# Optimization experiments

Hardware: AMD Instinct MI355X
Metric: run time of the kernel (lower is better)

Reference implementation:

```python
import jax, jax.numpy as jnp
import numpy as np

F, H, D, A, B = 500, 2000, 64, 64, 4096


def setup_inputs() -> dict:
    key = jax.random.key(0)
    ks = jax.random.split(key, 6)
    values = jax.random.normal(ks[0], (B, F), dtype=jnp.float32)
    feat_emb = jax.random.normal(ks[1], (F, D), dtype=jnp.float32) * 0.02
    hid_emb = jax.random.normal(ks[2], (H, D), dtype=jnp.float32) * 0.02
    Ww = jax.random.normal(ks[3], (2 * D, A), dtype=jnp.float32) * (1.0 / np.sqrt(2 * D))
    bw = jnp.zeros((A,), dtype=jnp.float32)
    Wu = jax.random.normal(ks[4], (A, 1), dtype=jnp.float32) * (1.0 / np.sqrt(A))
    mask = jax.random.bernoulli(ks[5], 0.1, (F, F + H, 1))
    return {"values": values, "feat_emb": feat_emb, "hid_emb": hid_emb,
            "Ww": Ww, "bw": bw, "Wu": Wu, "mask": mask}


def reference(values, feat_emb, hid_emb, Ww, bw, Wu, mask):
    d = feat_emb.shape[1]
    # full embedding matrix: concat(feature, hidden) -> [F+H, d]
    full = jnp.concatenate([feat_emb, hid_emb], axis=0)
    # Dense(tanh) on concat([feat_emb tiled, full tiled], axis=2) == split-weight form:
    # avoids materializing the [F, F+H, 2d] concat tensor (same math).
    W1, W2 = Ww[:d], Ww[d:]
    pre_f = feat_emb @ W1          # [F, A]
    pre_w = full @ W2              # [F+H, A]
    h = jnp.tanh(pre_f[:, None, :] + pre_w[None, :, :] + bw)  # [F, F+H, A]
    score = h @ Wu                 # [F, F+H, 1]
    # masked exp-normalize (not a stable softmax: original uses raw exp)
    score = jnp.where(mask, jnp.exp(score), 0.0)
    ssum = jnp.sum(score, axis=1, keepdims=True)        # [F, 1, 1]
    ssum = jnp.where(ssum == 0, 1.0, ssum)
    attn = score / ssum                                  # [F, F+H, 1]
    context = jnp.sum(attn * full[None, :, :], axis=1)   # [F, d]
    return values @ context                              # [B, d]
```

## Files before the change

kernel.cpp:

```cpp
#include <hip/hip_runtime.h>
#include <cstdint>
#include <cstddef>

#define F_N 500
#define H_N 2000
#define JN  2500
#define D_N 64
#define A_N 64
#define B_N 4096

#define SPLIT  2
#define JCHUNK 1250

__global__ __launch_bounds__(256) void k_pre(
    const float* __restrict__ feat, const float* __restrict__ hid,
    const float* __restrict__ Ww,   const float* __restrict__ bw,
    float* __restrict__ pre_f, float* __restrict__ pre_w,
    float* __restrict__ zero_region)
{
    const int gt = blockIdx.x * 256 + threadIdx.x;
    if (gt < 32512) zero_region[gt] = 0.0f;

    const int lane = threadIdx.x & 63;
    const int wave = threadIdx.x >> 6;
    int row = blockIdx.x * 4 + wave;
    row = __builtin_amdgcn_readfirstlane(row);
    if (row >= F_N + JN) return;

    const float* emb;
    const float* W;
    float*       outp;
    float acc0, acc1 = 0.0f;

    if (row < F_N) {
        emb  = feat + (size_t)row * D_N;
        W    = Ww;
        outp = pre_f + (size_t)row * A_N;
        acc0 = bw[lane];
    } else {
        const int j = row - F_N;
        emb  = (j < F_N) ? (feat + (size_t)j * D_N)
                         : (hid + (size_t)(j - F_N) * D_N);
        W    = Ww + D_N * A_N;
        outp = pre_w + (size_t)j * A_N;
        acc0 = 0.0f;
    }

    #pragma unroll
    for (int d = 0; d < D_N; d += 2) {
        acc0 = fmaf(emb[d],     W[(d    ) * A_N + lane], acc0);
        acc1 = fmaf(emb[d + 1], W[(d + 1) * A_N + lane], acc1);
    }
    outp[lane] = acc0 + acc1;
}

__global__ __launch_bounds__(256) void k_attn(
    const float* __restrict__ feat, const float* __restrict__ hid,
    const float* __restrict__ pre_f, const float* __restrict__ pre_w,
    const float* __restrict__ Wu,   const void* __restrict__ mask,
    float* __restrict__ csum, float* __restrict__ esum)
{
    const int tid  = threadIdx.x;
    const int lane = tid & 63;
    const int wave = tid >> 6;
    const int i    = blockIdx.x >> 1;
    const int sub  = blockIdx.x & 1;
    const int jbase = sub * JCHUNK;

    __shared__ int   list[JCHUNK];
    __shared__ float earr[JCHUNK];
    __shared__ float s_ctx[4][64];
    __shared__ int   nact;

    if (tid == 0) nact = 0;
    __syncthreads();

    const uint32_t* mw = (const uint32_t*)mask;
    const uint32_t probe = mw[lane] | mw[64 + lane] | mw[128 + lane] | mw[192 + lane];
    const bool byteMode = (__ballot(probe > 1u) != 0ull);

    const uint8_t*  mb = (const uint8_t*)mask + (size_t)i * JN + jbase;
    const uint32_t* mi = (const uint32_t*)mask + (size_t)i * JN + jbase;

    for (int t = tid; t < 1280; t += 256) {
        uint32_t m = 0;
        if (t < JCHUNK) m = byteMode ? (uint32_t)mb[t] : mi[t];
        const unsigned long long act = __ballot(m != 0);
        const int cnt = __popcll(act);
        int base = 0;
        if (lane == 0 && cnt) base = atomicAdd(&nact, cnt);
        base = __shfl(base, 0, 64);
        if (m) {
            const int rank = __popcll(act & ((1ull << lane) - 1ull));
            list[base + rank] = jbase + t;
        }
    }
    __syncthreads();
    const int n = nact;

    const float* pf = pre_f + (size_t)i * A_N;
    for (int idx = tid; idx < n; idx += 256) {
        const int j = list[idx];
        const float4* pwj = (const float4*)(pre_w + (size_t)j * A_N);
        float s = 0.0f;
        #pragma unroll
        for (int q = 0; q < 16; ++q) {
            const float4 v = pwj[q];
            const int a = q * 4;
            const float x0 = pf[a + 0] + v.x;
            const float x1 = pf[a + 1] + v.y;
            const float x2 = pf[a + 2] + v.z;
            const float x3 = pf[a + 3] + v.w;
            const float t0 = fmaf(-2.0f, __builtin_amdgcn_rcpf(__expf(2.0f * x0) + 1.0f), 1.0f);
            const float t1 = fmaf(-2.0f, __builtin_amdgcn_rcpf(__expf(2.0f * x1) + 1.0f), 1.0f);
            const float t2 = fmaf(-2.0f, __builtin_amdgcn_rcpf(__expf(2.0f * x2) + 1.0f), 1.0f);
            const float t3 = fmaf(-2.0f, __builtin_amdgcn_rcpf(__expf(2.0f * x3) + 1.0f), 1.0f);
            s = fmaf(Wu[a + 0], t0, s);
            s = fmaf(Wu[a + 1], t1, s);
            s = fmaf(Wu[a + 2], t2, s);
            s = fmaf(Wu[a + 3], t3, s);
        }
        earr[idx] = __expf(s);
    }
    __syncthreads();

    float cacc = 0.0f;
    int idx = wave;
    for (; idx + 12 < n; idx += 16) {
        const float e0 = earr[idx];      const int j0 = list[idx];
        const float e1 = earr[idx + 4];  const int j1 = list[idx + 4];
        const float e2 = earr[idx + 8];  const int j2 = list[idx + 8];
        const float e3 = earr[idx + 12]; const int j3 = list[idx + 12];
        const float* r0 = (j0 < F_N) ? (feat + (size_t)j0 * D_N) : (hid + (size_t)(j0 - F_N) * D_N);
        const float* r1 = (j1 < F_N) ? (feat + (size_t)j1 * D_N) : (hid + (size_t)(j1 - F_N) * D_N);
        const float* r2 = (j2 < F_N) ? (feat + (size_t)j2 * D_N) : (hid + (size_t)(j2 - F_N) * D_N);
        const float* r3 = (j3 < F_N) ? (feat + (size_t)j3 * D_N) : (hid + (size_t)(j3 - F_N) * D_N);
        const float v0 = r0[lane];
        const float v1 = r1[lane];
        const float v2 = r2[lane];
        const float v3 = r3[lane];
        cacc = fmaf(e0, v0, cacc);
        cacc = fmaf(e1, v1, cacc);
        cacc = fmaf(e2, v2, cacc);
        cacc = fmaf(e3, v3, cacc);
    }
    for (; idx < n; idx += 4) {
        const float e = earr[idx];
        const int   j = list[idx];
        const float* row = (j < F_N) ? (feat + (size_t)j * D_N)
                                     : (hid + (size_t)(j - F_N) * D_N);
        cacc = fmaf(e, row[lane], cacc);
    }
    s_ctx[wave][lane] = cacc;
    __syncthreads();

    if (wave == 0) {
        const float c4 = s_ctx[0][lane] + s_ctx[1][lane] + s_ctx[2][lane] + s_ctx[3][lane];
        float ss = 0.0f;
        for (int k = lane; k < n; k += 64) ss += earr[k];
        #pragma unroll
        for (int off = 1; off < 64; off <<= 1) ss += __shfl_xor(ss, off, 64);
        atomicAdd(&csum[(size_t)i * D_N + lane], c4);
        if (lane == 0) atomicAdd(&esum[i], ss);
    }
}

__global__ __launch_bounds__(256) void k_out(
    const float* __restrict__ values, const float* __restrict__ csum,
    const float* __restrict__ esum,   float* __restrict__ out)
{
    const int tid  = threadIdx.x;
    const int lane = tid & 63;
    const int wave = tid >> 6;
    int r0 = blockIdx.x * 8 + wave * 2;
    r0 = __builtin_amdgcn_readfirstlane(r0);

    __shared__ float ctx_l[100 * 64];

    float4 cbuf[7];
    float  ebuf[7];

    float acc0 = 0.0f, acc1 = 0.0f;

    {
        const float4* cp = (const float4*)csum;
        #pragma unroll
        for (int q = 0; q < 7; ++q) {
            const int t = tid + q * 256;
            if (t < 1600) { cbuf[q] = cp[t]; ebuf[q] = esum[t >> 4]; }
        }
    }

    for (int chunk = 0; chunk < 5; ++chunk) {
        __syncthreads();
        {
            float4* cl = (float4*)ctx_l;
            #pragma unroll
            for (int q = 0; q < 7; ++q) {
                const int t = tid + q * 256;
                if (t < 1600) {
                    const float e   = ebuf[q];
                    const float inv = (e == 0.0f) ? 1.0f : __builtin_amdgcn_rcpf(e);
                    float4 c = cbuf[q];
                    c.x *= inv; c.y *= inv; c.z *= inv; c.w *= inv;
                    cl[t] = c;
                }
            }
        }
        __syncthreads();

        if (chunk < 4) {
            const int k0n = (chunk + 1) * 100;
            const float4* cp = (const float4*)(csum + (size_t)k0n * 64);
            #pragma unroll
            for (int q = 0; q < 7; ++q) {
                const int t = tid + q * 256;
                if (t < 1600) { cbuf[q] = cp[t]; ebuf[q] = esum[k0n + (t >> 4)]; }
            }
        }

        const int k0 = chunk * 100;
        const float* v0 = values + (size_t)(r0 + 0) * 500 + k0;
        const float* v1 = values + (size_t)(r0 + 1) * 500 + k0;
        #pragma unroll 10
        for (int k = 0; k < 100; k += 4) {
            const float c0 = ctx_l[(k + 0) * 64 + lane];
            const float c1 = ctx_l[(k + 1) * 64 + lane];
            const float c2 = ctx_l[(k + 2) * 64 + lane];
            const float c3 = ctx_l[(k + 3) * 64 + lane];
            acc0 = fmaf(v0[k + 0], c0, acc0); acc0 = fmaf(v0[k + 1], c1, acc0);
            acc0 = fmaf(v0[k + 2], c2, acc0); acc0 = fmaf(v0[k + 3], c3, acc0);
            acc1 = fmaf(v1[k + 0], c0, acc1); acc1 = fmaf(v1[k + 1], c1, acc1);
            acc1 = fmaf(v1[k + 2], c2, acc1); acc1 = fmaf(v1[k + 3], c3, acc1);
        }
    }

    out[(size_t)(r0 + 0) * 64 + lane] = acc0;
    out[(size_t)(r0 + 1) * 64 + lane] = acc1;
}

extern "C" void kernel_launch(void* const* d_in, const int* in_sizes, int n_in,
                              void* d_out, int out_size, void* d_ws, size_t ws_size,
                              hipStream_t stream)
{
    const float* values = (const float*)d_in[0];
    const float* feat   = (const float*)d_in[1];
    const float* hid    = (const float*)d_in[2];
    const float* Ww     = (const float*)d_in[3];
    const float* bw     = (const float*)d_in[4];
    const float* Wu     = (const float*)d_in[5];
    const void*  mask   = d_in[6];
    float* out = (float*)d_out;

    float* wsf   = (float*)d_ws;
    float* pre_f = wsf;
    float* pre_w = wsf + 32000;
    float* csum  = wsf + 192000;
    float* esum  = wsf + 224000;

    k_pre <<<750,  256, 0, stream>>>(feat, hid, Ww, bw, pre_f, pre_w, csum);
    k_attn<<<1000, 256, 0, stream>>>(feat, hid, pre_f, pre_w, Wu, mask, csum, esum);
    k_out <<<512,  256, 0, stream>>>(values, csum, esum, out);
}
```

Measured before the change: 109.4 us.

## Fuse attention and output kernels into one launch with software grid barrier

After: 267.1 us. +144.2%, slower.

```diff
diff --git a/kernel.cpp b/kernel.cpp
--- a/kernel.cpp
+++ b/kernel.cpp
@@ -11,6 +11,7 @@
 
 #define SPLIT  2
 #define JCHUNK 1250
+#define NBLK   1000
 
 __global__ __launch_bounds__(256) void k_pre(
     const float* __restrict__ feat, const float* __restrict__ hid,
@@ -19,7 +20,7 @@
     float* __restrict__ zero_region)
 {
     const int gt = blockIdx.x * 256 + threadIdx.x;
-    if (gt < 32512) zero_region[gt] = 0.0f;
+    if (gt < 32514) zero_region[gt] = 0.0f;
 
     const int lane = threadIdx.x & 63;
     const int wave = threadIdx.x >> 6;
@@ -54,189 +55,218 @@
     outp[lane] = acc0 + acc1;
 }
 
-__global__ __launch_bounds__(256) void k_attn(
+__device__ __forceinline__ void grid_barrier(int* __restrict__ ctr,
+                                             int* __restrict__ gen,
+                                             int nblocks, bool wait)
+{
+    __syncthreads();
+    if (threadIdx.x == 0) {
+        __threadfence();
+        const int g = __hip_atomic_load(gen, __ATOMIC_RELAXED,
+                                        __HIP_MEMORY_SCOPE_AGENT);
+        const int old = __hip_atomic_fetch_add(ctr, 1, __ATOMIC_ACQ_REL,
+                                               __HIP_MEMORY_SCOPE_AGENT);
+        if (old == nblocks - 1) {
+            __hip_atomic_store(gen, g + 1, __ATOMIC_RELEASE,
+                               __HIP_MEMORY_SCOPE_AGENT);
+        } else if (wait) {
+            while (__hip_atomic_load(gen, __ATOMIC_ACQUIRE,
+                                     __HIP_MEMORY_SCOPE_AGENT) == g) {
+                __builtin_amdgcn_s_sleep(2);
+            }
+        }
+    }
+    if (wait) __syncthreads();
+}
+
+__global__ __launch_bounds__(256, 4) void k_mega(
     const float* __restrict__ feat, const float* __restrict__ hid,
     const float* __restrict__ pre_f, const float* __restrict__ pre_w,
     const float* __restrict__ Wu,   const void* __restrict__ mask,
-    float* __restrict__ csum, float* __restrict__ esum)
+    const float* __restrict__ values,
+    float* __restrict__ csum, float* __restrict__ esum,
+    float* __restrict__ out,  int* __restrict__ bar)
 {
     const int tid  = threadIdx.x;
     const int lane = tid & 63;
     const int wave = tid >> 6;
-    const int i    = blockIdx.x >> 1;
-    const int sub  = blockIdx.x & 1;
-    const int jbase = sub * JCHUNK;
-
-    __shared__ int   list[JCHUNK];
-    __shared__ float earr[JCHUNK];
-    __shared__ float s_ctx[4][64];
-    __shared__ int   nact;
-
-    if (tid == 0) nact = 0;
-    __syncthreads();
-
-    const uint32_t* mw = (const uint32_t*)mask;
-    const uint32_t probe = mw[lane] | mw[64 + lane] | mw[128 + lane] | mw[192 + lane];
-    const bool byteMode = (__ballot(probe > 1u) != 0ull);
-
-    const uint8_t*  mb = (const uint8_t*)mask + (size_t)i * JN + jbase;
-    const uint32_t* mi = (const uint32_t*)mask + (size_t)i * JN + jbase;
-
-    for (int t = tid; t < 1280; t += 256) {
-        uint32_t m = 0;
-        if (t < JCHUNK) m = byteMode ? (uint32_t)mb[t] : mi[t];
-        const unsigned long long act = __ballot(m != 0);
-        const int cnt = __popcll(act);
-        int base = 0;
-        if (lane == 0 && cnt) base = atomicAdd(&nact, cnt);
-        base = __shfl(base, 0, 64);
-        if (m) {
-            const int rank = __popcll(act & ((1ull << lane) - 1ull));
-            list[base + rank] = jbase + t;
-        }
-    }
-    __syncthreads();
-    const int n = nact;
-
-    const float* pf = pre_f + (size_t)i * A_N;
-    for (int idx = tid; idx < n; idx += 256) {
-        const int j = list[idx];
-        const float4* pwj = (const float4*)(pre_w + (size_t)j * A_N);
-        float s = 0.0f;
-        #pragma unroll
-        for (int q = 0; q < 16; ++q) {
-            const float4 v = pwj[q];
-            const int a = q * 4;
-            const float x0 = pf[a + 0] + v.x;
-            const float x1 = pf[a + 1] + v.y;
-            const float x2 = pf[a + 2] + v.z;
-            const float x3 = pf[a + 3] + v.w;
-            const float t0 = fmaf(-2.0f, __builtin_amdgcn_rcpf(__expf(2.0f * x0) + 1.0f), 1.0f);
-            const float t1 = fmaf(-2.0f, __builtin_amdgcn_rcpf(__expf(2.0f * x1) + 1.0f), 1.0f);
-            const float t2 = fmaf(-2.0f, __builtin_amdgcn_rcpf(__expf(2.0f * x2) + 1.0f), 1.0f);
-            const float t3 = fmaf(-2.0f, __builtin_amdgcn_rcpf(__expf(2.0f * x3) + 1.0f), 1.0f);
-            s = fmaf(Wu[a + 0], t0, s);
-            s = fmaf(Wu[a + 1], t1, s);
-            s = fmaf(Wu[a + 2], t2, s);
-            s = fmaf(Wu[a + 3], t3, s);
-        }
-        earr[idx] = __expf(s);
-    }
-    __syncthreads();
-
-    float cacc = 0.0f;
-    int idx = wave;
-    for (; idx + 12 < n; idx += 16) {
-        const float e0 = earr[idx];      const int j0 = list[idx];
-        const float e1 = earr[idx + 4];  const int j1 = list[idx + 4];
-        const float e2 = earr[idx + 8];  const int j2 = list[idx + 8];
-        const float e3 = earr[idx + 12]; const int j3 = list[idx + 12];
-        const float* r0 = (j0 < F_N) ? (feat + (size_t)j0 * D_N) : (hid + (size_t)(j0 - F_N) * D_N);
-        const float* r1 = (j1 < F_N) ? (feat + (size_t)j1 * D_N) : (hid + (size_t)(j1 - F_N) * D_N);
-        const float* r2 = (j2 < F_N) ? (feat + (size_t)j2 * D_N) : (hid + (size_t)(j2 - F_N) * D_N);
-        const float* r3 = (j3 < F_N) ? (feat + (size_t)j3 * D_N) : (hid + (size_t)(j3 - F_N) * D_N);
-        const float v0 = r0[lane];
-        const float v1 = r1[lane];
-        const float v2 = r2[lane];
-        const float v3 = r3[lane];
-        cacc = fmaf(e0, v0, cacc);
-        cacc = fmaf(e1, v1, cacc);
-        cacc = fmaf(e2, v2, cacc);
-        cacc = fmaf(e3, v3, cacc);
-    }
-    for (; idx < n; idx += 4) {
-        const float e = earr[idx];
-        const int   j = list[idx];
-        const float* row = (j < F_N) ? (feat + (size_t)j * D_N)
-                                     : (hid + (size_t)(j - F_N) * D_N);
-        cacc = fmaf(e, row[lane], cacc);
-    }
-    s_ctx[wave][lane] = cacc;
-    __syncthreads();
-
-    if (wave == 0) {
-        const float c4 = s_ctx[0][lane] + s_ctx[1][lane] + s_ctx[2][lane] + s_ctx[3][lane];
-        float ss = 0.0f;
-        for (int k = lane; k < n; k += 64) ss += earr[k];
-        #pragma unroll
-        for (int off = 1; off < 64; off <<= 1) ss += __shfl_xor(ss, off, 64);
-        atomicAdd(&csum[(size_t)i * D_N + lane], c4);
-        if (lane == 0) atomicAdd(&esum[i], ss);
-    }
-}
-
-__global__ __launch_bounds__(256) void k_out(
-    const float* __restrict__ values, const float* __restrict__ csum,
-    const float* __restrict__ esum,   float* __restrict__ out)
-{
-    const int tid  = threadIdx.x;
-    const int lane = tid & 63;
-    const int wave = tid >> 6;
-    int r0 = blockIdx.x * 8 + wave * 2;
-    r0 = __builtin_amdgcn_readfirstlane(r0);
-
-    __shared__ float ctx_l[100 * 64];
-
-    float4 cbuf[7];
-    float  ebuf[7];
-
-    float acc0 = 0.0f, acc1 = 0.0f;
+
+    __shared__ __align__(16) char smem[25600];
+    __shared__ int nact;
 
     {
-        const float4* cp = (const float4*)csum;
-        #pragma unroll
-        for (int q = 0; q < 7; ++q) {
-            const int t = tid + q * 256;
-            if (t < 1600) { cbuf[q] = cp[t]; ebuf[q] = esum[t >> 4]; }
-        }
-    }
-
-    for (int chunk = 0; chunk < 5; ++chunk) {
-        __syncthreads();
+        int*   list = (int*)smem;
+        float* earr = (float*)(smem + 5120);
+        float (*s_ctx)[64] = (float (*)[64])(smem + 10240);
+
+        const int i     = blockIdx.x >> 1;
+        const int sub   = blockIdx.x & 1;
+        const int jbase = sub * JCHUNK;
+
+        if (tid == 0) nact = 0;
+        __syncthreads();
+
+        const uint32_t* mw = (const uint32_t*)mask;
+        const uint32_t probe = mw[lane] | mw[64 + lane] | mw[128 + lane] | mw[192 + lane];
+        const bool byteMode = (__ballot(probe > 1u) != 0ull);
+
+        const uint8_t*  mb = (const uint8_t*)mask + (size_t)i * JN + jbase;
+        const uint32_t* mi = (const uint32_t*)mask + (size_t)i * JN + jbase;
+
+        for (int t = tid; t < 1280; t += 256) {
+            uint32_t m = 0;
+            if (t < JCHUNK) m = byteMode ? (uint32_t)mb[t] : mi[t];
+            const unsigned long long act = __ballot(m != 0);
+            const int cnt = __popcll(act);
+            int base = 0;
+            if (lane == 0 && cnt) base = atomicAdd(&nact, cnt);
+            base = __shfl(base, 0, 64);
+            if (m) {
+                const int rank = __popcll(act & ((1ull << lane) - 1ull));
+                list[base + rank] = jbase + t;
+            }
+        }
+        __syncthreads();
+        const int n = nact;
+
+        const float* pf = pre_f + (size_t)i * A_N;
+        for (int idx = tid; idx < n; idx += 256) {
+            const int j = list[idx];
+            const float4* pwj = (const float4*)(pre_w + (size_t)j * A_N);
+            float s = 0.0f;
+            #pragma unroll
+            for (int q = 0; q < 16; ++q) {
+                const float4 v = pwj[q];
+                const int a = q * 4;
+                const float x0 = pf[a + 0] + v.x;
+                const float x1 = pf[a + 1] + v.y;
+                const float x2 = pf[a + 2] + v.z;
+                const float x3 = pf[a + 3] + v.w;
+                const float t0 = fmaf(-2.0f, __builtin_amdgcn_rcpf(__expf(2.0f * x0) + 1.0f), 1.0f);
+                const float t1 = fmaf(-2.0f, __builtin_amdgcn_rcpf(__expf(2.0f * x1) + 1.0f), 1.0f);
+                const float t2 = fmaf(-2.0f, __builtin_amdgcn_rcpf(__expf(2.0f * x2) + 1.0f), 1.0f);
+                const float t3 = fmaf(-2.0f, __builtin_amdgcn_rcpf(__expf(2.0f * x3) + 1.0f), 1.0f);
+                s = fmaf(Wu[a + 0], t0, s);
+                s = fmaf(Wu[a + 1], t1, s);
+                s = fmaf(Wu[a + 2], t2, s);
+                s = fmaf(Wu[a + 3], t3, s);
+            }
+            earr[idx] = __expf(s);
+        }
+        __syncthreads();
+
+        float cacc = 0.0f;
+        int idx = wave;
+        for (; idx + 12 < n; idx += 16) {
+            const float e0 = earr[idx];      const int j0 = list[idx];
+            const float e1 = earr[idx + 4];  const int j1 = list[idx + 4];
+            const float e2 = earr[idx + 8];  const int j2 = list[idx + 8];
+            const float e3 = earr[idx + 12]; const int j3 = list[idx + 12];
+            const float* r0 = (j0 < F_N) ? (feat + (size_t)j0 * D_N) : (hid + (size_t)(j0 - F_N) * D_N);
+            const float* r1 = (j1 < F_N) ? (feat + (size_t)j1 * D_N) : (hid + (size_t)(j1 - F_N) * D_N);
+            const float* r2 = (j2 < F_N) ? (feat + (size_t)j2 * D_N) : (hid + (size_t)(j2 - F_N) * D_N);
+            const float* r3 = (j3 < F_N) ? (feat + (size_t)j3 * D_N) : (hid + (size_t)(j3 - F_N) * D_N);
+            const float v0 = r0[lane];
+            const float v1 = r1[lane];
+            const float v2 = r2[lane];
+            const float v3 = r3[lane];
+            cacc = fmaf(e0, v0, cacc);
+            cacc = fmaf(e1, v1, cacc);
+            cacc = fmaf(e2, v2, cacc);
+            cacc = fmaf(e3, v3, cacc);
+        }
+        for (; idx < n; idx += 4) {
+            const float e = earr[idx];
+            const int   j = list[idx];
+            const float* row = (j < F_N) ? (feat + (size_t)j * D_N)
+                                         : (hid + (size_t)(j - F_N) * D_N);
+            cacc = fmaf(e, row[lane], cacc);
+        }
+        s_ctx[wave][lane] = cacc;
+        __syncthreads();
+
+        if (wave == 0) {
+            const float c4 = s_ctx[0][lane] + s_ctx[1][lane] + s_ctx[2][lane] + s_ctx[3][lane];
+            float ss = 0.0f;
+            for (int k = lane; k < n; k += 64) ss += earr[k];
+            #pragma unroll
+            for (int off = 1; off < 64; off <<= 1) ss += __shfl_xor(ss, off, 64);
+            atomicAdd(&csum[(size_t)i * D_N + lane], c4);
+            if (lane == 0) atomicAdd(&esum[i], ss);
+        }
+    }
+
+    const bool doOut = (blockIdx.x < 512);
+    grid_barrier(bar + 0, bar + 1, NBLK, doOut);
+    if (!doOut) return;
+
+    {
+        float* ctx_l = (float*)smem;
+
+        int r0 = blockIdx.x * 8 + wave * 2;
+        r0 = __builtin_amdgcn_readfirstlane(r0);
+
+        float4 cbuf[7];
+        float  ebuf[7];
+
+        float acc0 = 0.0f, acc1 = 0.0f;
+
         {
-            float4* cl = (float4*)ctx_l;
+            const float4* cp = (const float4*)csum;
             #pragma unroll
             for (int q = 0; q < 7; ++q) {
                 const int t = tid + q * 256;
-                if (t < 1600) {
-                    const float e   = ebuf[q];
-                    const float inv = (e == 0.0f) ? 1.0f : __builtin_amdgcn_rcpf(e);
-                    float4 c = cbuf[q];
-                    c.x *= inv; c.y *= inv; c.z *= inv; c.w *= inv;
-                    cl[t] = c;
+                if (t < 1600) { cbuf[q] = cp[t]; ebuf[q] = esum[t >> 4]; }
+            }
+        }
+
+        for (int chunk = 0; chunk < 5; ++chunk) {
+            __syncthreads();
+            {
+                float4* cl = (float4*)ctx_l;
+                #pragma unroll
+                for (int q = 0; q < 7; ++q) {
+                    const int t = tid + q * 256;
+                    if (t < 1600) {
+                        const float e   = ebuf[q];
+                        const float inv = (e == 0.0f) ? 1.0f : __builtin_amdgcn_rcpf(e);
+                        float4 c = cbuf[q];
+                        c.x *= inv; c.y *= inv; c.z *= inv; c.w *= inv;
+                        cl[t] = c;
+                    }
                 }
             }
-        }
-        __syncthreads();
-
-        if (chunk < 4) {
-            const int k0n = (chunk + 1) * 100;
-            const float4* cp = (const float4*)(csum + (size_t)k0n * 64);
-            #pragma unroll
-            for (int q = 0; q < 7; ++q) {
-                const int t = tid + q * 256;
-                if (t < 1600) { cbuf[q] = cp[t]; ebuf[q] = esum[k0n + (t >> 4)]; }
-            }
-        }
-
-        const int k0 = chunk * 100;
-        const float* v0 = values + (size_t)(r0 + 0) * 500 + k0;
-        const float* v1 = values + (size_t)(r0 + 1) * 500 + k0;
-        #pragma unroll 10
-        for (int k = 0; k < 100; k += 4) {
-            const float c0 = ctx_l[(k + 0) * 64 + lane];
-            const float c1 = ctx_l[(k + 1) * 64 + lane];
-            const float c2 = ctx_l[(k + 2) * 64 + lane];
-            const float c3 = ctx_l[(k + 3) * 64 + lane];
-            acc0 = fmaf(v0[k + 0], c0, acc0); acc0 = fmaf(v0[k + 1], c1, acc0);
-            acc0 = fmaf(v0[k + 2], c2, acc0); acc0 = fmaf(v0[k + 3], c3, acc0);
-            acc1 = fmaf(v1[k + 0], c0, acc1); acc1 = fmaf(v1[k + 1], c1, acc1);
-            acc1 = fmaf(v1[k + 2], c2, acc1); acc1 = fmaf(v1[k + 3], c3, acc1);
-        }
-    }
-
-    out[(size_t)(r0 + 0) * 64 + lane] = acc0;
-    out[(size_t)(r0 + 1) * 64 + lane] = acc1;
+            __syncthreads();
+
+            if (chunk < 4) {
+                const int k0n = (chunk + 1) * 100;
+                const float4* cp = (const float4*)(csum + (size_t)k0n * 64);
+                #pragma unroll
+                for (int q = 0; q < 7; ++q) {
+                    const int t = tid + q * 256;
+                    if (t < 1600) { cbuf[q] = cp[t]; ebuf[q] = esum[k0n + (t >> 4)]; }
+                }
+            }
+
+            const int k0 = chunk * 100;
+            const float* v0 = values + (size_t)(r0 + 0) * 500 + k0;
+            const float* v1 = values + (size_t)(r0 + 1) * 500 + k0;
+            #pragma unroll 10
+            for (int k = 0; k < 100; k += 4) {
+                const float c0 = ctx_l[(k + 0) * 64 + lane];
+                const float c1 = ctx_l[(k + 1) * 64 + lane];
+                const float c2 = ctx_l[(k + 2) * 64 + lane];
+                const float c3 = ctx_l[(k + 3) * 64 + lane];
+                acc0 = fmaf(v0[k + 0], c0, acc0); acc0 = fmaf(v0[k + 1], c1, acc0);
+                acc0 = fmaf(v0[k + 2], c2, acc0); acc0 = fmaf(v0[k + 3], c3, acc0);
+                acc1 = fmaf(v1[k + 0], c0, acc1); acc1 = fmaf(v1[k + 1], c1, acc1);
+                acc1 = fmaf(v1[k + 2], c2, acc1); acc1 = fmaf(v1[k + 3], c3, acc1);
+            }
+        }
+
+        out[(size_t)(r0 + 0) * 64 + lane] = acc0;
+        out[(size_t)(r0 + 1) * 64 + lane] = acc1;
+    }
 }
 
 extern "C" void kernel_launch(void* const* d_in, const int* in_sizes, int n_in,
@@ -257,8 +287,9 @@
     float* pre_w = wsf + 32000;
     float* csum  = wsf + 192000;
     float* esum  = wsf + 224000;
+    int*   bar   = (int*)(wsf + 224512);
 
     k_pre <<<750,  256, 0, stream>>>(feat, hid, Ww, bw, pre_f, pre_w, csum);
-    k_attn<<<1000, 256, 0, stream>>>(feat, hid, pre_f, pre_w, Wu, mask, csum, esum);
-    k_out <<<512,  256, 0, stream>>>(values, csum, esum, out);
-}
+    k_mega<<<NBLK, 256, 0, stream>>>(feat, hid, pre_f, pre_w, Wu, mask,
+                                     values, csum, esum, out, bar);
+}
```
